# Performance work log

Measured on AMD Instinct MI355X. Metric: run time of the kernel, lower is better.

Reference implementation:

```python
import jax, jax.numpy as jnp
import numpy as np

N_NODES = 50000
N_EDGES = 800000
IN_C, HID_C, OUT_C = 128, 128, 64
BN_EPS = 1e-5


def setup_inputs() -> dict:
    key = jax.random.key(0)
    ks = jax.random.split(key, 12)
    def lin(k, fan_in, fan_out):
        bound = 1.0 / np.sqrt(fan_in)
        kw, kb = jax.random.split(k)
        W = jax.random.uniform(kw, (fan_in, fan_out), jnp.float32, -bound, bound)
        b = jax.random.uniform(kb, (fan_out,), jnp.float32, -bound, bound)
        return W, b
    x = jax.random.normal(ks[0], (N_NODES, IN_C), jnp.float32)
    edge_index = jax.random.randint(ks[1], (2, N_EDGES), 0, N_NODES, jnp.int32)
    w1a, b1a = lin(ks[2], IN_C, HID_C)
    w1b, b1b = lin(ks[3], HID_C, HID_C)
    w2a, b2a = lin(ks[4], HID_C, OUT_C)
    w2b, b2b = lin(ks[5], OUT_C, OUT_C)
    return {
        "x": x, "edge_index": edge_index,
        "w1a": w1a, "b1a": b1a, "g1": jnp.ones((HID_C,)), "be1": jnp.zeros((HID_C,)),
        "w1b": w1b, "b1b": b1b,
        "w2a": w2a, "b2a": b2a, "g2": jnp.ones((OUT_C,)), "be2": jnp.zeros((OUT_C,)),
        "w2b": w2b, "b2b": b2b,
    }


def _batchnorm(h, gamma, beta):
    # training-style BN over node dim, biased variance (torch BatchNorm1d)
    mean = jnp.mean(h, axis=0)
    var = jnp.mean(jnp.square(h - mean), axis=0)
    return (h - mean) * jax.lax.rsqrt(var + BN_EPS) * gamma + beta


def _gin_layer(x, src, dst, n_nodes, w_a, b_a, gamma, beta, w_b, b_b):
    # GINConv with eps=0: MLP(x + sum_{j->i} x_j)
    agg = jax.ops.segment_sum(x[src], dst, num_segments=n_nodes)  # [N, C]
    h = x + agg
    h = h @ w_a + b_a
    h = jax.nn.relu(_batchnorm(h, gamma, beta))
    return h @ w_b + b_b


def reference(x, edge_index, w1a, b1a, g1, be1, w1b, b1b, w2a, b2a, g2, be2, w2b, b2b):
    src, dst = edge_index[0], edge_index[1]
    n = x.shape[0]
    h = _gin_layer(x, src, dst, n, w1a, b1a, g1, be1, w1b, b1b)
    h = jax.nn.relu(h)  # dropout p=0.0 -> identity
    h = _gin_layer(h, src, dst, n, w2a, b2a, g2, be2, w2b, b2b)
    return jax.nn.log_softmax(h, axis=-1)
```

## Files before the change

### kernel.cpp

```cpp
#include <hip/hip_runtime.h>


typedef unsigned short u16;
typedef __attribute__((ext_vector_type(8))) short short8;
typedef __attribute__((ext_vector_type(4))) short short4v;
typedef __attribute__((ext_vector_type(4))) float f32x4;

#define DEV_INLINE __device__ __forceinline__

DEV_INLINE void atomAddF(float* p, float v) { unsafeAtomicAdd(p, v); }

DEV_INLINE u16 f2bf(float f) {
    unsigned u = __float_as_uint(f);
    u += 0x7fffu + ((u >> 16) & 1u);
    return (u16)(u >> 16);
}
DEV_INLINE float bf2f(u16 h) { return __uint_as_float(((unsigned)h) << 16); }

__global__ __launch_bounds__(256) void wprep_k(const float* __restrict__ W,
                                               short* __restrict__ wf,
                                               int K, int NOUT)
{
    const int units = (NOUT / 16) * (K / 32) * 64;
    const int u = blockIdx.x * 256 + threadIdx.x;
    if (u >= units) return;
    const int per_ct = (K / 32) * 64;
    const int ct = u / per_ct;
    const int rem = u % per_ct;
    const int kc = rem >> 6;
    const int l = rem & 63;
    const int col = ct * 16 + (l & 15);
    const int k0 = kc * 32 + (l >> 4) * 8;
    short8 pk;
#pragma unroll
    for (int j = 0; j < 8; j++)
        pk[j] = (short)f2bf(W[(size_t)(k0 + j) * NOUT + col]);
    *(short8*)&wf[(size_t)u * 8] = pk;
}

template <int KD, int NC, bool ABF16, bool BNIN, bool BIAS, bool RELUOUT,
          bool LOGSM, bool OBF16>
__global__ __launch_bounds__(256) void mgemm(
    const void* __restrict__ Ap, const short* __restrict__ Wf,
    const float* __restrict__ sc, const float* __restrict__ sh,
    const float* __restrict__ bias, void* __restrict__ outp, int M)
{
    constexpr int BM = 128;
    constexpr int KC = KD / 32;
    constexpr int CT = NC / 16;
    __shared__ short Asl[BM * KD];
    __shared__ short Bsl[NC * KD];

    const int t = threadIdx.x;
    const int l = t & 63;
    const int w = t >> 6;

    {
        const float4* src = (const float4*)Wf;
        float4* dst = (float4*)Bsl;
        constexpr int NU = NC * KD / 8;
#pragma unroll
        for (int u = t; u < NU; u += 256) dst[u] = src[u];
    }
    {
        const int r = t >> 1;
        const int half = t & 1;
        const int grow = blockIdx.x * BM + r;
        const int rt = r >> 4;
        constexpr int KH = KD / 2;
        u16 hv[KH];
        if (grow < M) {
            if constexpr (ABF16) {
                const u16* ap = (const u16*)Ap + (size_t)grow * KD + half * KH;
#pragma unroll
                for (int i = 0; i < KH / 8; i++)
                    *(short8*)&hv[i * 8] = ((const short8*)ap)[i];
                if constexpr (BNIN) {
#pragma unroll
                    for (int i = 0; i < KH; i++) {
                        const int k = half * KH + i;
                        hv[i] = f2bf(fmaxf(0.f, bf2f(hv[i]) * sc[k] + sh[k]));
                    }
                }
            } else {
                const float* ap = (const float*)Ap + (size_t)grow * KD + half * KH;
#pragma unroll
                for (int i = 0; i < KH / 4; i++) {
                    const float4 v = ((const float4*)ap)[i];
                    float f0 = v.x, f1 = v.y, f2 = v.z, f3 = v.w;
                    if constexpr (BNIN) {
                        const int k = half * KH + i * 4;
                        f0 = fmaxf(0.f, f0 * sc[k + 0] + sh[k + 0]);
                        f1 = fmaxf(0.f, f1 * sc[k + 1] + sh[k + 1]);
                        f2 = fmaxf(0.f, f2 * sc[k + 2] + sh[k + 2]);
                        f3 = fmaxf(0.f, f3 * sc[k + 3] + sh[k + 3]);
                    }
                    hv[i * 4 + 0] = f2bf(f0); hv[i * 4 + 1] = f2bf(f1);
                    hv[i * 4 + 2] = f2bf(f2); hv[i * 4 + 3] = f2bf(f3);
                }
            }
        } else {
#pragma unroll
            for (int i = 0; i < KH; i++) hv[i] = 0;
        }
#pragma unroll
        for (int g = 0; g < KH / 8; g++) {
            const int k0 = half * KH + g * 8;
            const int kc = k0 >> 5;
            const int lane = (r & 15) + ((k0 >> 3) & 3) * 16;
            *(short8*)&Asl[((rt * KC + kc) * 64 + lane) * 8] =
                *(short8*)&hv[g * 8];
        }
    }
    __syncthreads();

    const int rt0 = w * 2;
    f32x4 acc[2][CT];
#pragma unroll
    for (int i = 0; i < 2; i++)
#pragma unroll
        for (int c = 0; c < CT; c++) acc[i][c] = (f32x4){0.f, 0.f, 0.f, 0.f};

#pragma unroll
    for (int kc = 0; kc < KC; kc++) {
        const short8 x0 = *(const short8*)&Asl[((rt0 * KC + kc) * 64 + l) * 8];
        const short8 x1 = *(const short8*)&Asl[(((rt0 + 1) * KC + kc) * 64 + l) * 8];
#pragma unroll
        for (int ct = 0; ct < CT; ct++) {
            const short8 wb = *(const short8*)&Bsl[((ct * KC + kc) * 64 + l) * 8];
            acc[0][ct] = __builtin_amdgcn_mfma_f32_16x16x32_bf16(wb, x0, acc[0][ct], 0, 0, 0);
            acc[1][ct] = __builtin_amdgcn_mfma_f32_16x16x32_bf16(wb, x1, acc[1][ct], 0, 0, 0);
        }
    }

    const int cbase = (l >> 4) * 4;
#pragma unroll
    for (int rr = 0; rr < 2; rr++) {
        const int grow = blockIdx.x * BM + (rt0 + rr) * 16 + (l & 15);
        if constexpr (!LOGSM) {
            if (grow < M) {
#pragma unroll
                for (int ct = 0; ct < CT; ct++) {
                    f32x4 o = acc[rr][ct];
                    if constexpr (BIAS) {
                        const float4 bv = *(const float4*)&bias[ct * 16 + cbase];
                        o[0] += bv.x; o[1] += bv.y; o[2] += bv.z; o[3] += bv.w;
                    }
                    if constexpr (RELUOUT) {
#pragma unroll
                        for (int j = 0; j < 4; j++) o[j] = fmaxf(o[j], 0.f);
                    }
                    if constexpr (OBF16) {
                        short4v o16;
#pragma unroll
                        for (int j = 0; j < 4; j++) o16[j] = (short)f2bf(o[j]);
                        *(short4v*)&((u16*)outp)[(size_t)grow * NC + ct * 16 + cbase] = o16;
                    } else {
                        *(f32x4*)&((float*)outp)[(size_t)grow * NC + ct * 16 + cbase] = o;
                    }
                }
            }
        } else {
            float v[CT * 4];
#pragma unroll
            for (int ct = 0; ct < CT; ct++) {
                const float4 bv = *(const float4*)&bias[ct * 16 + cbase];
                v[ct * 4 + 0] = acc[rr][ct][0] + bv.x;
                v[ct * 4 + 1] = acc[rr][ct][1] + bv.y;
                v[ct * 4 + 2] = acc[rr][ct][2] + bv.z;
                v[ct * 4 + 3] = acc[rr][ct][3] + bv.w;
            }
            float m = v[0];
#pragma unroll
            for (int j = 1; j < CT * 4; j++) m = fmaxf(m, v[j]);
            m = fmaxf(m, __shfl_xor(m, 16));
            m = fmaxf(m, __shfl_xor(m, 32));
            float s = 0.f;
#pragma unroll
            for (int j = 0; j < CT * 4; j++) s += __expf(v[j] - m);
            s += __shfl_xor(s, 16);
            s += __shfl_xor(s, 32);
            const float lg = m + __logf(s);
            if (grow < M) {
#pragma unroll
                for (int ct = 0; ct < CT; ct++) {
                    f32x4 o;
#pragma unroll
                    for (int j = 0; j < 4; j++) o[j] = v[ct * 4 + j] - lg;
                    *(f32x4*)&((float*)outp)[(size_t)grow * NC + ct * 16 + cbase] = o;
                }
            }
        }
    }
}

__global__ __launch_bounds__(256) void hist_k(const int* __restrict__ ei,
                                              int* __restrict__ cnt, int E)
{
    const int gid = blockIdx.x * blockDim.x + threadIdx.x;
    const int stride = gridDim.x * blockDim.x;
    for (int e = gid; e < E; e += stride) atomicAdd(&cnt[ei[E + e]], 1);
}

__global__ __launch_bounds__(256) void bsum_k(const int* __restrict__ cnt,
                                              int* __restrict__ bsum, int N)
{
    __shared__ int ws[4];
    const int i = blockIdx.x * 256 + threadIdx.x;
    int v = (i < N) ? cnt[i] : 0;
    for (int d = 32; d; d >>= 1) v += __shfl_xor(v, d, 64);
    if ((threadIdx.x & 63) == 0) ws[threadIdx.x >> 6] = v;
    __syncthreads();
    if (threadIdx.x == 0) bsum[blockIdx.x] = ws[0] + ws[1] + ws[2] + ws[3];
}

__global__ __launch_bounds__(256) void bscan_k(const int* __restrict__ bsum,
                                               int* __restrict__ bpre, int G1)
{
    __shared__ int part[256];
    const int t = threadIdx.x;
    const int v = (t < G1) ? bsum[t] : 0;
    part[t] = v;
    __syncthreads();
    for (int d = 1; d < 256; d <<= 1) {
        const int u = (t >= d) ? part[t - d] : 0;
        __syncthreads();
        part[t] += u;
        __syncthreads();
    }
    bpre[t] = part[t] - v;
}

__global__ __launch_bounds__(256) void offs_k(const int* __restrict__ cnt,
                                              const int* __restrict__ bpre,
                                              int* __restrict__ off,
                                              int* __restrict__ cursor,
                                              int N, int E)
{
    __shared__ int part[256];
    const int t = threadIdx.x;
    const int i = blockIdx.x * 256 + t;
    const int v = (i < N) ? cnt[i] : 0;
    part[t] = v;
    __syncthreads();
    for (int d = 1; d < 256; d <<= 1) {
        const int u = (t >= d) ? part[t - d] : 0;
        __syncthreads();
        part[t] += u;
        __syncthreads();
    }
    if (i < N) {
        const int o = bpre[blockIdx.x] + part[t] - v;
        off[i] = o;
        cursor[i] = o;
    }
    if (blockIdx.x == 0 && t == 0) off[N] = E;
}

__global__ __launch_bounds__(256) void fill_k(const int* __restrict__ ei,
                                              int* __restrict__ cursor,
                                              int* __restrict__ srcs, int E)
{
    const int gid = blockIdx.x * blockDim.x + threadIdx.x;
    const int stride = gridDim.x * blockDim.x;
    for (int e = gid; e < E; e += stride) {
        const int s = ei[e];
        const int d = ei[E + e];
        const int pos = atomicAdd(&cursor[d], 1);
        srcs[pos] = s;
    }
}

template <int C>
__global__ __launch_bounds__(256) void segsum_bf(
    const u16* __restrict__ p, const int* __restrict__ off,
    const int* __restrict__ srcs, u16* __restrict__ out,
    float* __restrict__ sum, float* __restrict__ sumsq, int N)
{
    constexpr int NPG  = 256 / C;
    constexpr int BLKN = 16;
    __shared__ float red[256];

    const int slot = threadIdx.x / C;
    const int c = threadIdx.x % C;
    const int base = blockIdx.x * (NPG * BLKN);
    float ssum = 0.f, ssq = 0.f;

    for (int i = 0; i < BLKN; i++) {
        const int n = base + i * NPG + slot;
        if (n < N) {
            const int lo = off[n], hi = off[n + 1];
            float acc = bf2f(p[(size_t)n * C + c]);
            int e = lo;
            for (; e + 3 < hi; e += 4) {
                const int s0 = srcs[e], s1 = srcs[e + 1];
                const int s2 = srcs[e + 2], s3 = srcs[e + 3];
                const float v0 = bf2f(p[(size_t)s0 * C + c]);
                const float v1 = bf2f(p[(size_t)s1 * C + c]);
                const float v2 = bf2f(p[(size_t)s2 * C + c]);
                const float v3 = bf2f(p[(size_t)s3 * C + c]);
                acc += v0; acc += v1; acc += v2; acc += v3;
            }
            for (; e < hi; e++) acc += bf2f(p[(size_t)srcs[e] * C + c]);
            const u16 r = f2bf(acc);
            out[(size_t)n * C + c] = r;
            const float rf = bf2f(r);
            ssum += rf;
            ssq += rf * rf;
        }
    }
    if (slot > 0) red[threadIdx.x] = ssum;
    __syncthreads();
    if (slot == 0) {
#pragma unroll
        for (int s = 1; s < NPG; s++) ssum += red[s * C + c];
    }
    __syncthreads();
    if (slot > 0) red[threadIdx.x] = ssq;
    __syncthreads();
    if (slot == 0) {
#pragma unroll
        for (int s = 1; s < NPG; s++) ssq += red[s * C + c];
        atomAddF(&sum[c], ssum);
        atomAddF(&sumsq[c], ssq);
    }
}

__global__ void bnfinal_k(const float* __restrict__ sum,
                          const float* __restrict__ sumsq,
                          const float* __restrict__ g,
                          const float* __restrict__ be,
                          float* __restrict__ sc, float* __restrict__ sh,
                          int C, float invN)
{
    const int c = threadIdx.x;
    if (c < C) {
        const float m = sum[c] * invN;
        const float v = sumsq[c] * invN - m * m;
        const float r = rsqrtf(v + 1e-5f);
        const float s = g[c] * r;
        sc[c] = s;
        sh[c] = be[c] - m * s;
    }
}

extern "C" void kernel_launch(void* const* d_in, const int* in_sizes, int n_in,
                              void* d_out, int out_size, void* d_ws, size_t ws_size,
                              hipStream_t stream)
{
    const float* x   = (const float*)d_in[0];
    const int*   ei  = (const int*)d_in[1];
    const float* w1a = (const float*)d_in[2];
    const float* g1  = (const float*)d_in[4];
    const float* be1 = (const float*)d_in[5];
    const float* w1b = (const float*)d_in[6];
    const float* b1b = (const float*)d_in[7];
    const float* w2a = (const float*)d_in[8];
    const float* g2  = (const float*)d_in[10];
    const float* be2 = (const float*)d_in[11];
    const float* w2b = (const float*)d_in[12];
    const float* b2b = (const float*)d_in[13];
    float* out = (float*)d_out;

    const int N = in_sizes[0] / 128;
    const int E = in_sizes[1] / 2;

    u16* buf1 = (u16*)d_ws;
    u16* buf2 = buf1 + (size_t)N * 128;
    float* stats = (float*)(buf2 + (size_t)N * 128);
    float* sum1 = stats,       *sq1 = stats + 128;
    float* sum2 = stats + 256, *sq2 = stats + 320;
    float* sc1  = stats + 384, *sh1 = stats + 512;
    float* sc2  = stats + 640, *sh2 = stats + 704;
    int* cnt    = (int*)(stats + 1024);
    int* off    = cnt + N;
    int* cursor = off + N + 1;
    int* srcs   = cursor + N;
    int* bsum   = srcs + E;
    int* bpre   = bsum + 256;
    short* w1af = (short*)(bpre + 256);
    short* w1bf = w1af + 128 * 128;
    short* w2af = w1bf + 128 * 128;
    short* w2bf = w2af + 128 * 64;
    u16* p1 = buf1;
    u16* s1 = buf2;
    u16* h1 = buf1;
    u16* p2 = buf2;
    u16* s2 = buf2 + (size_t)N * 64;

    hipMemsetAsync(stats, 0, 1024 * sizeof(float) + (size_t)N * sizeof(int), stream);

    const int G1 = (N + 255) / 256;
    const int gb = (N + 127) / 128;
    const int gs128 = (N + 31) / 32;
    const int gs64  = (N + 63) / 64;

    hist_k<<<1024, 256, 0, stream>>>(ei, cnt, E);
    bsum_k<<<G1, 256, 0, stream>>>(cnt, bsum, N);
    bscan_k<<<1, 256, 0, stream>>>(bsum, bpre, G1);
    offs_k<<<G1, 256, 0, stream>>>(cnt, bpre, off, cursor, N, E);
    fill_k<<<1024, 256, 0, stream>>>(ei, cursor, srcs, E);

    wprep_k<<<8, 256, 0, stream>>>(w1a, w1af, 128, 128);
    wprep_k<<<8, 256, 0, stream>>>(w1b, w1bf, 128, 128);
    wprep_k<<<4, 256, 0, stream>>>(w2a, w2af, 128, 64);
    wprep_k<<<2, 256, 0, stream>>>(w2b, w2bf, 64, 64);

    mgemm<128, 128, false, false, false, false, false, true>
        <<<gb, 256, 0, stream>>>(x, w1af, nullptr, nullptr, nullptr, p1, N);
    segsum_bf<128><<<gs128, 256, 0, stream>>>(p1, off, srcs, s1, sum1, sq1, N);
    bnfinal_k<<<1, 128, 0, stream>>>(sum1, sq1, g1, be1, sc1, sh1, 128, 1.f / N);
    mgemm<128, 128, true, true, true, true, false, true>
        <<<gb, 256, 0, stream>>>(s1, w1bf, sc1, sh1, b1b, h1, N);

    mgemm<128, 64, true, false, false, false, false, true>
        <<<gb, 256, 0, stream>>>(h1, w2af, nullptr, nullptr, nullptr, p2, N);
    segsum_bf<64><<<gs64, 256, 0, stream>>>(p2, off, srcs, s2, sum2, sq2, N);
    bnfinal_k<<<1, 64, 0, stream>>>(sum2, sq2, g2, be2, sc2, sh2, 64, 1.f / N);
    mgemm<64, 64, true, true, true, false, true, false>
        <<<gb, 256, 0, stream>>>(s2, w2bf, sc2, sh2, b2b, out, N);
}
```

Baseline: 338.3 us.

## Map one wavefront per node in CSR gather and merge weight-prep launches

The segment-sum kernel now gives each destination node one whole wavefront, with lanes covering channels. For C=128 each lane loads two bf16 values as one 32-bit word. Edge offsets are made wave-uniform with readfirstlane, and source indices are prefetched eight at a time in a software pipeline so the dependent gathers issue without waiting on index loads. The partial statistics are reduced through a single shared-memory pass, and the four weight-prep launches are merged into one kernel. The aim is to raise memory-level parallelism and widen accesses in the gather, which is latency-bound. The cost is extra padded loads on the final edge batch of each node, plus idle lanes on low-degree nodes.

```diff
diff --git a/kernel.cpp b/kernel.cpp
--- a/kernel.cpp
+++ b/kernel.cpp
@@ -2,6 +2,7 @@
 
 
 typedef unsigned short u16;
+typedef unsigned int u32;
 typedef __attribute__((ext_vector_type(8))) short short8;
 typedef __attribute__((ext_vector_type(4))) short short4v;
 typedef __attribute__((ext_vector_type(4))) float f32x4;
@@ -17,12 +18,20 @@
 }
 DEV_INLINE float bf2f(u16 h) { return __uint_as_float(((unsigned)h) << 16); }
 
-__global__ __launch_bounds__(256) void wprep_k(const float* __restrict__ W,
-                                               short* __restrict__ wf,
-                                               int K, int NOUT)
-{
+__global__ __launch_bounds__(256) void wprep4_k(
+    const float* __restrict__ w1a, const float* __restrict__ w1b,
+    const float* __restrict__ w2a, const float* __restrict__ w2b,
+    short* __restrict__ o1a, short* __restrict__ o1b,
+    short* __restrict__ o2a, short* __restrict__ o2b)
+{
+    int b = blockIdx.x;
+    const float* W; short* wf; int K, NOUT;
+    if (b < 8)       { W = w1a; wf = o1a; K = 128; NOUT = 128; }
+    else if (b < 16) { W = w1b; wf = o1b; K = 128; NOUT = 128; b -= 8; }
+    else if (b < 20) { W = w2a; wf = o2a; K = 128; NOUT = 64;  b -= 16; }
+    else             { W = w2b; wf = o2b; K = 64;  NOUT = 64;  b -= 20; }
+    const int u = b * 256 + threadIdx.x;
     const int units = (NOUT / 16) * (K / 32) * 64;
-    const int u = blockIdx.x * 256 + threadIdx.x;
     if (u >= units) return;
     const int per_ct = (K / 32) * 64;
     const int ct = u / per_ct;
@@ -277,52 +286,95 @@
     const int* __restrict__ srcs, u16* __restrict__ out,
     float* __restrict__ sum, float* __restrict__ sumsq, int N)
 {
-    constexpr int NPG  = 256 / C;
-    constexpr int BLKN = 16;
-    __shared__ float red[256];
-
-    const int slot = threadIdx.x / C;
-    const int c = threadIdx.x % C;
-    const int base = blockIdx.x * (NPG * BLKN);
-    float ssum = 0.f, ssq = 0.f;
+    constexpr int BLKN = 8;
+    constexpr int VPL = C / 64;
+    __shared__ float red[4][64][2 * VPL];
+
+    const int wv = threadIdx.x >> 6;
+    const int l  = threadIdx.x & 63;
+    const int base = blockIdx.x * 4 * BLKN;
+
+    float ss[VPL], qq[VPL];
+#pragma unroll
+    for (int v = 0; v < VPL; v++) { ss[v] = 0.f; qq[v] = 0.f; }
 
     for (int i = 0; i < BLKN; i++) {
-        const int n = base + i * NPG + slot;
+        const int n = base + i * 4 + wv;
         if (n < N) {
-            const int lo = off[n], hi = off[n + 1];
-            float acc = bf2f(p[(size_t)n * C + c]);
-            int e = lo;
-            for (; e + 3 < hi; e += 4) {
-                const int s0 = srcs[e], s1 = srcs[e + 1];
-                const int s2 = srcs[e + 2], s3 = srcs[e + 3];
-                const float v0 = bf2f(p[(size_t)s0 * C + c]);
-                const float v1 = bf2f(p[(size_t)s1 * C + c]);
-                const float v2 = bf2f(p[(size_t)s2 * C + c]);
-                const float v3 = bf2f(p[(size_t)s3 * C + c]);
-                acc += v0; acc += v1; acc += v2; acc += v3;
-            }
-            for (; e < hi; e++) acc += bf2f(p[(size_t)srcs[e] * C + c]);
-            const u16 r = f2bf(acc);
-            out[(size_t)n * C + c] = r;
-            const float rf = bf2f(r);
-            ssum += rf;
-            ssq += rf * rf;
-        }
-    }
-    if (slot > 0) red[threadIdx.x] = ssum;
+            const int lo = __builtin_amdgcn_readfirstlane(off[n]);
+            const int hi = __builtin_amdgcn_readfirstlane(off[n + 1]);
+            float acc[VPL];
+            if constexpr (VPL == 2) {
+                const u32 u = *(const u32*)&p[(size_t)n * C + 2 * l];
+                acc[0] = bf2f((u16)u);
+                acc[1] = bf2f((u16)(u >> 16));
+            } else {
+                acc[0] = bf2f(p[(size_t)n * C + l]);
+            }
+            const int cnt = hi - lo;
+            if (cnt > 0) {
+                const int last = hi - 1;
+                int idx[8];
+#pragma unroll
+                for (int j = 0; j < 8; j++) idx[j] = srcs[min(lo + j, last)];
+                for (int e = lo; e < hi; e += 8) {
+                    int nx[8];
+#pragma unroll
+                    for (int j = 0; j < 8; j++)
+                        nx[j] = srcs[min(e + 8 + j, last)];
+#pragma unroll
+                    for (int j = 0; j < 8; j++) {
+                        const bool live = (e + j) < hi;
+                        if constexpr (VPL == 2) {
+                            const u32 u = *(const u32*)&p[(size_t)idx[j] * C + 2 * l];
+                            const float v0 = bf2f((u16)u);
+                            const float v1 = bf2f((u16)(u >> 16));
+                            acc[0] += live ? v0 : 0.f;
+                            acc[1] += live ? v1 : 0.f;
+                        } else {
+                            const float v = bf2f(p[(size_t)idx[j] * C + l]);
+                            acc[0] += live ? v : 0.f;
+                        }
+                    }
+#pragma unroll
+                    for (int j = 0; j < 8; j++) idx[j] = nx[j];
+                }
+            }
+            if constexpr (VPL == 2) {
+                const u16 r0 = f2bf(acc[0]);
+                const u16 r1 = f2bf(acc[1]);
+                *(u32*)&out[(size_t)n * C + 2 * l] = (u32)r0 | ((u32)r1 << 16);
+                const float f0 = bf2f(r0), f1 = bf2f(r1);
+                ss[0] += f0; qq[0] += f0 * f0;
+                ss[1] += f1; qq[1] += f1 * f1;
+            } else {
+                const u16 r = f2bf(acc[0]);
+                out[(size_t)n * C + l] = r;
+                const float f = bf2f(r);
+                ss[0] += f; qq[0] += f * f;
+            }
+        }
+    }
+
+#pragma unroll
+    for (int v = 0; v < VPL; v++) {
+        red[wv][l][2 * v] = ss[v];
+        red[wv][l][2 * v + 1] = qq[v];
+    }
     __syncthreads();
-    if (slot == 0) {
-#pragma unroll
-        for (int s = 1; s < NPG; s++) ssum += red[s * C + c];
-    }
-    __syncthreads();
-    if (slot > 0) red[threadIdx.x] = ssq;
-    __syncthreads();
-    if (slot == 0) {
-#pragma unroll
-        for (int s = 1; s < NPG; s++) ssq += red[s * C + c];
-        atomAddF(&sum[c], ssum);
-        atomAddF(&sumsq[c], ssq);
+    if (wv == 0) {
+#pragma unroll
+        for (int v = 0; v < VPL; v++) {
+            float a = 0.f, b = 0.f;
+#pragma unroll
+            for (int w2 = 0; w2 < 4; w2++) {
+                a += red[w2][l][2 * v];
+                b += red[w2][l][2 * v + 1];
+            }
+            const int ch = (VPL == 2) ? (2 * l + v) : l;
+            atomAddF(&sum[ch], a);
+            atomAddF(&sumsq[ch], b);
+        }
     }
 }
 
@@ -392,8 +444,7 @@
 
     const int G1 = (N + 255) / 256;
     const int gb = (N + 127) / 128;
-    const int gs128 = (N + 31) / 32;
-    const int gs64  = (N + 63) / 64;
+    const int gs = (N + 31) / 32;
 
     hist_k<<<1024, 256, 0, stream>>>(ei, cnt, E);
     bsum_k<<<G1, 256, 0, stream>>>(cnt, bsum, N);
@@ -401,21 +452,18 @@
     offs_k<<<G1, 256, 0, stream>>>(cnt, bpre, off, cursor, N, E);
     fill_k<<<1024, 256, 0, stream>>>(ei, cursor, srcs, E);
 
-    wprep_k<<<8, 256, 0, stream>>>(w1a, w1af, 128, 128);
-    wprep_k<<<8, 256, 0, stream>>>(w1b, w1bf, 128, 128);
-    wprep_k<<<4, 256, 0, stream>>>(w2a, w2af, 128, 64);
-    wprep_k<<<2, 256, 0, stream>>>(w2b, w2bf, 64, 64);
+    wprep4_k<<<22, 256, 0, stream>>>(w1a, w1b, w2a, w2b, w1af, w1bf, w2af, w2bf);
 
     mgemm<128, 128, false, false, false, false, false, true>
         <<<gb, 256, 0, stream>>>(x, w1af, nullptr, nullptr, nullptr, p1, N);
-    segsum_bf<128><<<gs128, 256, 0, stream>>>(p1, off, srcs, s1, sum1, sq1, N);
+    segsum_bf<128><<<gs, 256, 0, stream>>>(p1, off, srcs, s1, sum1, sq1, N);
     bnfinal_k<<<1, 128, 0, stream>>>(sum1, sq1, g1, be1, sc1, sh1, 128, 1.f / N);
     mgemm<128, 128, true, true, true, true, false, true>
         <<<gb, 256, 0, stream>>>(s1, w1bf, sc1, sh1, b1b, h1, N);
 
     mgemm<128, 64, true, false, false, false, false, true>
         <<<gb, 256, 0, stream>>>(h1, w2af, nullptr, nullptr, nullptr, p2, N);
-    segsum_bf<64><<<gs64, 256, 0, stream>>>(p2, off, srcs, s2, sum2, sq2, N);
+    segsum_bf<64><<<gs, 256, 0, stream>>>(p2, off, srcs, s2, sum2, sq2, N);
     bnfinal_k<<<1, 64, 0, stream>>>(sum2, sq2, g2, be2, sc2, sh2, 64, 1.f / N);
     mgemm<64, 64, true, true, true, false, true, false>
         <<<gb, 256, 0, stream>>>(s2, w2bf, sc2, sh2, b2b, out, N);
```

New measurement: 309.1 us. 8.6% less time.
